# Kernel optimization log

Measured on AMD Instinct MI355X. Metric: run time of the kernel, lower is better.

Reference implementation:

```python
import jax, jax.numpy as jnp
import numpy as np

K = 9          # kernel_size
PAD = K // 2   # same padding
SIGMA = 1.0
EPS = 1e-5     # BatchNorm eps


def setup_inputs() -> dict:
    key = jax.random.key(0)
    k0, k1, k2 = jax.random.split(key, 3)
    B, Cin, Cout, L = 4, 64, 64, 131072
    x = jax.random.normal(k0, (B, Cin, L), jnp.float32)
    coords = jax.random.uniform(k1, (B, 3, L), jnp.float32)  # 3D point coords in [0,1)
    W = jax.random.normal(k2, (Cout, Cin, K), jnp.float32) * (1.0 / np.sqrt(Cin * K))
    bias = jnp.zeros((Cout,), jnp.float32)
    gamma = jnp.ones((Cout,), jnp.float32)
    beta = jnp.zeros((Cout,), jnp.float32)
    return {"x": x, "coords": coords, "W": W, "bias": bias, "gamma": gamma, "beta": beta}


def reference(x, coords, W, bias, gamma, beta):
    B, Cin, L = x.shape
    # zero-pad sequence dim for 'same' conv
    xpad = jnp.pad(x, ((0, 0), (0, 0), (PAD, PAD)))
    cpad = jnp.pad(coords, ((0, 0), (0, 0), (PAD, PAD)))
    # unfold: neighbor windows of size K (K is a small compile-time constant)
    x_unf = jnp.stack([xpad[:, :, k:k + L] for k in range(K)], axis=2)   # [B,Cin,K,L]
    c_unf = jnp.stack([cpad[:, :, k:k + L] for k in range(K)], axis=2)   # [B,3,K,L]
    # Gaussian spatial weights from coord distances (WeightedConv1D)
    dist2 = jnp.sum((c_unf - coords[:, :, None, :]) ** 2, axis=1)        # [B,K,L]
    w = jnp.exp(-dist2 / (2.0 * SIGMA * SIGMA))                          # [B,K,L]
    # weighted conv: contract over (Cin, K)
    out = jnp.einsum('ock,bckl->bol', W, x_unf * w[:, None, :, :])       # [B,Cout,L]
    out = out + bias[None, :, None]
    # BatchNorm1d (training-mode batch statistics over B and L) + ReLU
    mean = out.mean(axis=(0, 2), keepdims=True)
    var = out.var(axis=(0, 2), keepdims=True)
    out = (out - mean) * jax.lax.rsqrt(var + EPS)
    out = out * gamma[None, :, None] + beta[None, :, None]
    return jax.nn.relu(out)
```

## Files before the change

kernel.cpp:

```cpp
#include <hip/hip_runtime.h>
#include <hip/hip_bf16.h>

#define KK 9
#define PADK 4
#define CIN 64
#define COUT 64
#define LSEQ 131072
#define NB 4
#define TILE 64
#define XROWS 72
#define XRS 72
#define NTILES 2048
#define NPART 64

typedef __attribute__((ext_vector_type(8))) short v8s;
typedef __attribute__((ext_vector_type(4))) float v4f;

__device__ __forceinline__ unsigned short f2bf(float f) {
  __hip_bfloat16 h = __float2bfloat16(f);
  return *reinterpret_cast<unsigned short*>(&h);
}
__device__ __forceinline__ float bf2f(unsigned short s) {
  return __uint_as_float(((unsigned)s) << 16);
}

__device__ __forceinline__ void store_o(float* p, float v) { *p = v; }
__device__ __forceinline__ void store_o(__hip_bfloat16* p, float v) { *p = __float2bfloat16(v); }

__global__ void wtrans_kernel(const float* __restrict__ W, v8s* __restrict__ Wt) {
  int t = blockIdx.x * 256 + threadIdx.x;
  if (t >= KK * 2 * 4 * 64) return;
  int lane = t & 63;
  int frag = t >> 6;
  int mblk = frag & 3;
  int s    = (frag >> 2) & 1;
  int k    = frag >> 3;
  int m = lane & 15, q = lane >> 4;
  int o = mblk * 16 + m;
  union { v8s v; unsigned short h[8]; } u;
#pragma unroll
  for (int j = 0; j < 8; ++j) {
    int c = 32 * s + q * 8 + j;
    u.h[j] = f2bf(W[(o * CIN + c) * KK + k]);
  }
  Wt[t] = u.v;
}

template <typename OutT>
__global__ __launch_bounds__(256, 5)
void conv_kernel(const float* __restrict__ x, const float* __restrict__ coords,
                 const v8s* __restrict__ Wt, OutT* __restrict__ cv,
                 float* __restrict__ stat_sum, float* __restrict__ stat_sq) {
  __shared__ __align__(16) __hip_bfloat16 xt[XROWS][XRS];
  __shared__ float wt[KK][TILE];

  const int tid  = threadIdx.x;
  const int wv   = tid >> 6;
  const int lane = tid & 63;
  const int gw   = blockIdx.x;
  const int b    = gw >> 11;
  const int tile = gw & (NTILES - 1);
  const int l0   = tile * TILE;
  const float* xb = x + (b * CIN) * LSEQ;
  const float* cb = coords + (b * 3) * LSEQ;
  const int m = lane & 15;
  const int q = lane >> 4;

  {
    int mm = tid & 15;
    int c4 = (tid >> 4) * 4;
    float4 f[4];
#pragma unroll
    for (int t = 0; t < 4; ++t)
      f[t] = *(const float4*)(xb + (c4 + t) * LSEQ + l0 + 4 * mm);
    const float* fp = (const float*)&f[0];
#pragma unroll
    for (int j = 0; j < 4; ++j) {
      union { unsigned long long v; unsigned short h[4]; } u;
#pragma unroll
      for (int t = 0; t < 4; ++t) u.h[t] = f2bf(fp[4 * t + j]);
      *(unsigned long long*)&xt[4 + 4 * mm + j][c4] = u.v;
    }
  }
  if (tid < 128) {
    int side = tid >> 6;
    int c = tid & 63;
    if (side == 0) {
      float el[4] = {0.f, 0.f, 0.f, 0.f};
      if (tile != 0) {
#pragma unroll
        for (int j = 0; j < 4; ++j) el[j] = xb[c * LSEQ + l0 - 4 + j];
      }
#pragma unroll
      for (int j = 0; j < 4; ++j) xt[j][c] = __float2bfloat16(el[j]);
    } else {
      float er[4] = {0.f, 0.f, 0.f, 0.f};
      if (tile != NTILES - 1) {
#pragma unroll
        for (int j = 0; j < 4; ++j) er[j] = xb[c * LSEQ + l0 + TILE + j];
      }
#pragma unroll
      for (int j = 0; j < 4; ++j) xt[68 + j][c] = __float2bfloat16(er[j]);
    }
  }
  if (tid < 64) {
    int n = tid;
    float sx = cb[l0 + n];
    float sy = cb[LSEQ + l0 + n];
    float sz = cb[2 * LSEQ + l0 + n];
    float w9[KK];
#pragma unroll
    for (int k = 0; k < KK; ++k) {
      int l = l0 + n + k - PADK;
      float cx = 0.f, cy = 0.f, cz = 0.f;
      if ((unsigned)l < (unsigned)LSEQ) {
        cx = cb[l]; cy = cb[LSEQ + l]; cz = cb[2 * LSEQ + l];
      }
      float dx = cx - sx, dy = cy - sy, dz = cz - sz;
      w9[k] = __expf(-0.5f * (dx * dx + dy * dy + dz * dz));
    }
#pragma unroll
    for (int k = 0; k < KK; ++k)
      wt[k][n] = w9[k] - ((k < KK - 1) ? w9[k + 1] : 0.f);
  }
  __syncthreads();

  v4f y[4], tot[4];
#pragma unroll
  for (int j = 0; j < 4; ++j) {
    y[j]   = (v4f){0.f, 0.f, 0.f, 0.f};
    tot[j] = (v4f){0.f, 0.f, 0.f, 0.f};
  }

  const v8s* wp = Wt + wv * 64 + lane;
  v8s a0 = wp[0];
  v8s a1 = wp[256];

#pragma unroll 1
  for (int k = 0; k < KK; ++k) {
#pragma unroll
    for (int nbq = 0; nbq < 4; ++nbq) {
      const __hip_bfloat16* rowp = &xt[nbq * 16 + m + k][q * 8];
      v8s b0 = *(const v8s*)(rowp);
      v8s b1 = *(const v8s*)(rowp + 32);
      y[nbq] = __builtin_amdgcn_mfma_f32_16x16x32_bf16(a0, b0, y[nbq], 0, 0, 0);
      y[nbq] = __builtin_amdgcn_mfma_f32_16x16x32_bf16(a1, b1, y[nbq], 0, 0, 0);
    }
    int kn = k + (k < KK - 1);
    a0 = wp[kn * 512];
    a1 = wp[kn * 512 + 256];
#pragma unroll
    for (int nbq = 0; nbq < 4; ++nbq) {
      float d = wt[k][nbq * 16 + m];
#pragma unroll
      for (int r = 0; r < 4; ++r)
        tot[nbq][r] = __builtin_fmaf(d, y[nbq][r], tot[nbq][r]);
    }
  }

  const int part = gw & (NPART - 1);
  OutT* outb = cv + (b * COUT) * LSEQ;
#pragma unroll
  for (int r = 0; r < 4; ++r) {
    int o = wv * 16 + q * 4 + r;
    float s1 = 0.f, s2 = 0.f;
#pragma unroll
    for (int nbq = 0; nbq < 4; ++nbq) {
      float v = tot[nbq][r];
      s1 += v;
      s2 += v * v;
      store_o(&outb[o * LSEQ + l0 + nbq * 16 + m], v);
    }
#pragma unroll
    for (int off = 1; off < 16; off <<= 1) {
      s1 += __shfl_xor(s1, off, 64);
      s2 += __shfl_xor(s2, off, 64);
    }
    if (m == 0) {
      atomicAdd(&stat_sum[part * COUT + o], s1);
      atomicAdd(&stat_sq [part * COUT + o], s2);
    }
  }
}

__global__ void finalize_kernel(const float* __restrict__ stat_sum,
                                const float* __restrict__ stat_sq,
                                const float* __restrict__ gamma,
                                const float* __restrict__ beta,
                                float* __restrict__ ss) {
  int o = threadIdx.x;
  float s1 = 0.f, s2 = 0.f;
  for (int p = 0; p < NPART; ++p) {
    s1 += stat_sum[p * COUT + o];
    s2 += stat_sq [p * COUT + o];
  }
  const float invN = 1.0f / (float)(NB * LSEQ);
  float mean = s1 * invN;
  float var  = s2 * invN - mean * mean;
  float sc = gamma[o] * rsqrtf(var + 1e-5f);
  ss[o]        = sc;
  ss[COUT + o] = beta[o] - mean * sc;
}

__global__ __launch_bounds__(256)
void scale_f32_kernel(float* __restrict__ data, const float* __restrict__ ss) {
  const int blk = blockIdx.x;
  const int ch = (blk >> 6) & 63;
  const float sc = ss[ch];
  const float sh = ss[COUT + ch];
  const int base = blk * 2048 + threadIdx.x * 8;
  float4 a = *(float4*)(data + base);
  float4 b = *(float4*)(data + base + 4);
  a.x = fmaxf(fmaf(a.x, sc, sh), 0.f);
  a.y = fmaxf(fmaf(a.y, sc, sh), 0.f);
  a.z = fmaxf(fmaf(a.z, sc, sh), 0.f);
  a.w = fmaxf(fmaf(a.w, sc, sh), 0.f);
  b.x = fmaxf(fmaf(b.x, sc, sh), 0.f);
  b.y = fmaxf(fmaf(b.y, sc, sh), 0.f);
  b.z = fmaxf(fmaf(b.z, sc, sh), 0.f);
  b.w = fmaxf(fmaf(b.w, sc, sh), 0.f);
  *(float4*)(data + base)     = a;
  *(float4*)(data + base + 4) = b;
}

__global__ __launch_bounds__(256)
void scale_bf16_kernel(const __hip_bfloat16* __restrict__ cvin,
                       const float* __restrict__ ss, float* __restrict__ out) {
  const int blk = blockIdx.x;
  const int ch = (blk >> 6) & 63;
  const float sc = ss[ch];
  const float sh = ss[COUT + ch];
  const int base = blk * 2048 + threadIdx.x * 8;
  union { v8s v; unsigned short h[8]; } u;
  u.v = *(const v8s*)(cvin + base);
  float r[8];
#pragma unroll
  for (int i = 0; i < 8; ++i)
    r[i] = fmaxf(fmaf(bf2f(u.h[i]), sc, sh), 0.f);
  *(float4*)(out + base)     = make_float4(r[0], r[1], r[2], r[3]);
  *(float4*)(out + base + 4) = make_float4(r[4], r[5], r[6], r[7]);
}

extern "C" void kernel_launch(void* const* d_in, const int* in_sizes, int n_in,
                              void* d_out, int out_size, void* d_ws, size_t ws_size,
                              hipStream_t stream) {
  const float* x      = (const float*)d_in[0];
  const float* coords = (const float*)d_in[1];
  const float* W      = (const float*)d_in[2];
  const float* gamma  = (const float*)d_in[4];
  const float* beta   = (const float*)d_in[5];
  float* out = (float*)d_out;
  char* ws = (char*)d_ws;

  float* stat_sum = (float*)(ws);
  float* stat_sq  = (float*)(ws + 16384);
  float* ss       = (float*)(ws + 32768);
  v8s*   Wt       = (v8s*)(ws + 40960);
  __hip_bfloat16* scratch = (__hip_bfloat16*)(ws + 131072);

  const size_t need_bf16 = (size_t)131072 + (size_t)NB * COUT * LSEQ * 2;
  const bool bf16_path = ws_size >= need_bf16;

  hipMemsetAsync(ws, 0, 32768, stream);
  wtrans_kernel<<<18, 256, 0, stream>>>(W, Wt);

  if (bf16_path) {
    conv_kernel<__hip_bfloat16><<<NB * NTILES, 256, 0, stream>>>(
        x, coords, Wt, scratch, stat_sum, stat_sq);
    finalize_kernel<<<1, COUT, 0, stream>>>(stat_sum, stat_sq, gamma, beta, ss);
    scale_bf16_kernel<<<(NB * COUT * (LSEQ / 2048)), 256, 0, stream>>>(scratch, ss, out);
  } else {
    conv_kernel<float><<<NB * NTILES, 256, 0, stream>>>(
        x, coords, Wt, out, stat_sum, stat_sq);
    finalize_kernel<<<1, COUT, 0, stream>>>(stat_sum, stat_sq, gamma, beta, ss);
    scale_f32_kernel<<<(NB * COUT * (LSEQ / 2048)), 256, 0, stream>>>(out, ss);
  }
}
```

Baseline: 322.6 us.

## Double conv tile length and split waves over output-channel and position blocks

```diff
diff --git a/kernel.cpp b/kernel.cpp
--- a/kernel.cpp
+++ b/kernel.cpp
@@ -7,10 +7,10 @@
 #define COUT 64
 #define LSEQ 131072
 #define NB 4
-#define TILE 64
-#define XROWS 72
+#define TILEL 128
+#define XROWS 136
 #define XRS 72
-#define NTILES 2048
+#define NTILES 1024
 #define NPART 64
 
 typedef __attribute__((ext_vector_type(8))) short v8s;
@@ -47,39 +47,42 @@
 }
 
 template <typename OutT>
-__global__ __launch_bounds__(256, 5)
+__global__ __launch_bounds__(256, 4)
 void conv_kernel(const float* __restrict__ x, const float* __restrict__ coords,
                  const v8s* __restrict__ Wt, OutT* __restrict__ cv,
                  float* __restrict__ stat_sum, float* __restrict__ stat_sq) {
   __shared__ __align__(16) __hip_bfloat16 xt[XROWS][XRS];
-  __shared__ float wt[KK][TILE];
+  __shared__ float wt[KK][TILEL];
 
   const int tid  = threadIdx.x;
   const int wv   = tid >> 6;
+  const int wo   = wv & 1;
+  const int wl   = wv >> 1;
   const int lane = tid & 63;
   const int gw   = blockIdx.x;
-  const int b    = gw >> 11;
+  const int b    = gw >> 10;
   const int tile = gw & (NTILES - 1);
-  const int l0   = tile * TILE;
+  const int l0   = tile * TILEL;
   const float* xb = x + (b * CIN) * LSEQ;
   const float* cb = coords + (b * 3) * LSEQ;
   const int m = lane & 15;
   const int q = lane >> 4;
 
   {
-    int mm = tid & 15;
-    int c4 = (tid >> 4) * 4;
-    float4 f[4];
-#pragma unroll
-    for (int t = 0; t < 4; ++t)
-      f[t] = *(const float4*)(xb + (c4 + t) * LSEQ + l0 + 4 * mm);
+    int cg = tid & 7;
+    int lc = tid >> 3;
+    int c8 = cg * 8;
+    float4 f[8];
+#pragma unroll
+    for (int t = 0; t < 8; ++t)
+      f[t] = *(const float4*)(xb + (c8 + t) * LSEQ + l0 + 4 * lc);
     const float* fp = (const float*)&f[0];
 #pragma unroll
     for (int j = 0; j < 4; ++j) {
-      union { unsigned long long v; unsigned short h[4]; } u;
-#pragma unroll
-      for (int t = 0; t < 4; ++t) u.h[t] = f2bf(fp[4 * t + j]);
-      *(unsigned long long*)&xt[4 + 4 * mm + j][c4] = u.v;
+      union { v8s v; unsigned short h[8]; } u;
+#pragma unroll
+      for (int t = 0; t < 8; ++t) u.h[t] = f2bf(fp[4 * t + j]);
+      *(v8s*)&xt[4 + 4 * lc + j][c8] = u.v;
     }
   }
   if (tid < 128) {
@@ -97,13 +100,13 @@
       float er[4] = {0.f, 0.f, 0.f, 0.f};
       if (tile != NTILES - 1) {
 #pragma unroll
-        for (int j = 0; j < 4; ++j) er[j] = xb[c * LSEQ + l0 + TILE + j];
-      }
-#pragma unroll
-      for (int j = 0; j < 4; ++j) xt[68 + j][c] = __float2bfloat16(er[j]);
-    }
-  }
-  if (tid < 64) {
+        for (int j = 0; j < 4; ++j) er[j] = xb[c * LSEQ + l0 + TILEL + j];
+      }
+#pragma unroll
+      for (int j = 0; j < 4; ++j) xt[128 + 4 + j][c] = __float2bfloat16(er[j]);
+    }
+  }
+  if (tid < TILEL) {
     int n = tid;
     float sx = cb[l0 + n];
     float sy = cb[LSEQ + l0 + n];
@@ -125,60 +128,65 @@
   }
   __syncthreads();
 
-  v4f y[4], tot[4];
-#pragma unroll
-  for (int j = 0; j < 4; ++j) {
-    y[j]   = (v4f){0.f, 0.f, 0.f, 0.f};
-    tot[j] = (v4f){0.f, 0.f, 0.f, 0.f};
-  }
-
-  const v8s* wp = Wt + wv * 64 + lane;
-  v8s a0 = wp[0];
-  v8s a1 = wp[256];
+  v4f y[2][4], tot[2][4];
+#pragma unroll
+  for (int i = 0; i < 2; ++i)
+#pragma unroll
+    for (int j = 0; j < 4; ++j) {
+      y[i][j]   = (v4f){0.f, 0.f, 0.f, 0.f};
+      tot[i][j] = (v4f){0.f, 0.f, 0.f, 0.f};
+    }
+
+  const v8s* wp = Wt + (wo * 2) * 64 + lane;
 
 #pragma unroll 1
   for (int k = 0; k < KK; ++k) {
 #pragma unroll
+    for (int s = 0; s < 2; ++s) {
+      v8s a0 = wp[k * 512 + s * 256];
+      v8s a1 = wp[k * 512 + s * 256 + 64];
+#pragma unroll
+      for (int nbq = 0; nbq < 4; ++nbq) {
+        v8s bf = *(const v8s*)&xt[wl * 64 + nbq * 16 + m + k][q * 8 + 32 * s];
+        y[0][nbq] = __builtin_amdgcn_mfma_f32_16x16x32_bf16(a0, bf, y[0][nbq], 0, 0, 0);
+        y[1][nbq] = __builtin_amdgcn_mfma_f32_16x16x32_bf16(a1, bf, y[1][nbq], 0, 0, 0);
+      }
+    }
+#pragma unroll
     for (int nbq = 0; nbq < 4; ++nbq) {
-      const __hip_bfloat16* rowp = &xt[nbq * 16 + m + k][q * 8];
-      v8s b0 = *(const v8s*)(rowp);
-      v8s b1 = *(const v8s*)(rowp + 32);
-      y[nbq] = __builtin_amdgcn_mfma_f32_16x16x32_bf16(a0, b0, y[nbq], 0, 0, 0);
-      y[nbq] = __builtin_amdgcn_mfma_f32_16x16x32_bf16(a1, b1, y[nbq], 0, 0, 0);
-    }
-    int kn = k + (k < KK - 1);
-    a0 = wp[kn * 512];
-    a1 = wp[kn * 512 + 256];
-#pragma unroll
-    for (int nbq = 0; nbq < 4; ++nbq) {
-      float d = wt[k][nbq * 16 + m];
-#pragma unroll
-      for (int r = 0; r < 4; ++r)
-        tot[nbq][r] = __builtin_fmaf(d, y[nbq][r], tot[nbq][r]);
+      float d = wt[k][wl * 64 + nbq * 16 + m];
+#pragma unroll
+      for (int mb = 0; mb < 2; ++mb)
+#pragma unroll
+        for (int r = 0; r < 4; ++r)
+          tot[mb][nbq][r] = __builtin_fmaf(d, y[mb][nbq][r], tot[mb][nbq][r]);
     }
   }
 
   const int part = gw & (NPART - 1);
   OutT* outb = cv + (b * COUT) * LSEQ;
 #pragma unroll
-  for (int r = 0; r < 4; ++r) {
-    int o = wv * 16 + q * 4 + r;
-    float s1 = 0.f, s2 = 0.f;
-#pragma unroll
-    for (int nbq = 0; nbq < 4; ++nbq) {
-      float v = tot[nbq][r];
-      s1 += v;
-      s2 += v * v;
-      store_o(&outb[o * LSEQ + l0 + nbq * 16 + m], v);
-    }
-#pragma unroll
-    for (int off = 1; off < 16; off <<= 1) {
-      s1 += __shfl_xor(s1, off, 64);
-      s2 += __shfl_xor(s2, off, 64);
-    }
-    if (m == 0) {
-      atomicAdd(&stat_sum[part * COUT + o], s1);
-      atomicAdd(&stat_sq [part * COUT + o], s2);
+  for (int mb = 0; mb < 2; ++mb) {
+#pragma unroll
+    for (int r = 0; r < 4; ++r) {
+      int o = wo * 32 + mb * 16 + q * 4 + r;
+      float s1 = 0.f, s2 = 0.f;
+#pragma unroll
+      for (int nbq = 0; nbq < 4; ++nbq) {
+        float v = tot[mb][nbq][r];
+        s1 += v;
+        s2 += v * v;
+        store_o(&outb[o * LSEQ + l0 + wl * 64 + nbq * 16 + m], v);
+      }
+#pragma unroll
+      for (int off = 1; off < 16; off <<= 1) {
+        s1 += __shfl_xor(s1, off, 64);
+        s2 += __shfl_xor(s2, off, 64);
+      }
+      if (m == 0) {
+        atomicAdd(&stat_sum[part * COUT + o], s1);
+        atomicAdd(&stat_sq [part * COUT + o], s2);
+      }
     }
   }
 }
```

Measured after the change: 321.0 us. Within noise of the previous version (-0.5%).
